# Kernel tuning notes

Hardware: AMD Instinct MI355X
Metric: run time of the kernel (lower is better)

Reference implementation:

```python
import jax, jax.numpy as jnp
import numpy as np

B, N, C = 16, 4096, 64
M, K, R = 1024, 32, 0.2
EPS = 1e-5  # BatchNorm eps (eval mode: running_mean=0, running_var=1)


def setup_inputs() -> dict:
    key = jax.random.key(0)
    ks = jax.random.split(key, 8)
    s = 0.05
    return {
        "points": jax.random.normal(ks[0], (B, 3, N), dtype=jnp.float32),
        "features": jax.random.normal(ks[1], (B, C, N), dtype=jnp.float32),
        "w1": jax.random.normal(ks[2], (64, 3 + C), dtype=jnp.float32) * s,
        "b1": jnp.zeros((64,), jnp.float32),
        "g1": jnp.ones((64,), jnp.float32),
        "be1": jnp.zeros((64,), jnp.float32),
        "w2": jax.random.normal(ks[3], (64, 64), dtype=jnp.float32) * s,
        "b2": jnp.zeros((64,), jnp.float32),
        "g2": jnp.ones((64,), jnp.float32),
        "be2": jnp.zeros((64,), jnp.float32),
        "w3": jax.random.normal(ks[4], (128, 64), dtype=jnp.float32) * s,
        "b3": jnp.zeros((128,), jnp.float32),
        "g3": jnp.ones((128,), jnp.float32),
        "be3": jnp.zeros((128,), jnp.float32),
    }


def farthest_point_sampling(pts, m):
    """pts: [B,N,3] -> indices [B,m] (iterative FPS, first point = index 0)."""
    b, n, _ = pts.shape

    def step(carry, _):
        dist, last = carry  # dist [b,n], last [b]
        lastp = jnp.take_along_axis(pts, last[:, None, None], axis=1)  # [b,1,3]
        d = jnp.sum((pts - lastp) ** 2, axis=-1)  # [b,n]
        dist = jnp.minimum(dist, d)
        nxt = jnp.argmax(dist, axis=1).astype(jnp.int32)
        return (dist, nxt), last

    init = (jnp.full((b, n), 1e10, pts.dtype), jnp.zeros((b,), jnp.int32))
    _, idx = jax.lax.scan(step, init, None, length=m)
    return idx.T  # [b,m]


def ball_query(pts, centroids, k, radius):
    """pts [B,N,3], centroids [B,M,3] -> neighbor indices [B,M,K].
    Takes the first k points (by index) within radius; pads with the first hit,
    matching the PointNet++ CUDA ball_query semantics."""
    n = pts.shape[1]
    p2 = jnp.sum(pts ** 2, -1)  # [B,N]
    c2 = jnp.sum(centroids ** 2, -1)  # [B,M]
    d2 = c2[:, :, None] + p2[:, None, :] - 2.0 * jnp.einsum("bmd,bnd->bmn", centroids, pts)
    ar = jnp.arange(n, dtype=jnp.int32)
    key = jnp.where(d2 <= radius * radius, ar[None, None, :], n)  # [B,M,N]
    idx = jnp.sort(key, axis=-1)[..., :k]  # first k in-radius indices (or n)
    first = idx[..., :1]  # centroid itself is always a hit (d2=0)
    idx = jnp.where(idx < n, idx, first)
    return jnp.clip(idx, 0, n - 1)


def _mlp_block(x, w, bias, g, be):
    # 1x1 Conv2d + BatchNorm (eval: mean=0, var=1) + ReLU, x: [B,M,K,Cin]
    y = jnp.einsum("oc,bmkc->bmko", w, x) + bias
    y = y * (g / jnp.sqrt(1.0 + EPS)) + be
    return jax.nn.relu(y)


def reference(points, features, w1, b1, g1, be1, w2, b2, g2, be2, w3, b3, g3, be3):
    pts = jnp.transpose(points, (0, 2, 1))  # [B,N,3]
    feats = jnp.transpose(features, (0, 2, 1))  # [B,N,C]
    b = pts.shape[0]

    cidx = farthest_point_sampling(pts, M)  # [B,M]
    bidx = jnp.arange(b)[:, None]
    cent = pts[bidx, cidx]  # [B,M,3]

    nidx = ball_query(pts, cent, K, R)  # [B,M,K]
    bidx2 = jnp.arange(b)[:, None, None]
    gpts = pts[bidx2, nidx]  # [B,M,K,3]
    gfeat = feats[bidx2, nidx]  # [B,M,K,C]
    local = gpts - cent[:, :, None, :]  # local coords
    x = jnp.concatenate([local, gfeat], axis=-1)  # [B,M,K,3+C]

    x = _mlp_block(x, w1, b1, g1, be1)
    x = _mlp_block(x, w2, b2, g2, be2)
    x = _mlp_block(x, w3, b3, g3, be3)

    out = jnp.max(x, axis=2)  # max over K samples -> [B,M,Cout]
    centroids = jnp.transpose(cent, (0, 2, 1))  # [B,3,M]
    out = jnp.transpose(out, (0, 2, 1))  # [B,Cout,M]
    return centroids, out
```

## Files before the change

kernel.cpp:

```cpp
#include <hip/hip_runtime.h>
#include <math.h>

#define NPTS 4096
#define MC   1024
#define KNB  32

typedef __attribute__((ext_vector_type(8))) short bf16x8;
typedef __attribute__((ext_vector_type(4))) float f32x4;

__device__ __forceinline__ unsigned short f2bf(float f) {
  unsigned int u = __float_as_uint(f);
  u = u + 0x7fffu + ((u >> 16) & 1u);
  return (unsigned short)(u >> 16);
}

template <int CTRL>
__device__ __forceinline__ unsigned long long dpp_kmax(unsigned long long k) {
  int lo = (int)(unsigned int)k;
  int hi = (int)(unsigned int)(k >> 32);
  int lo2 = __builtin_amdgcn_update_dpp(lo, lo, CTRL, 0xF, 0xF, false);
  int hi2 = __builtin_amdgcn_update_dpp(hi, hi, CTRL, 0xF, 0xF, false);
  unsigned long long k2 =
      ((unsigned long long)(unsigned int)hi2 << 32) | (unsigned int)lo2;
  return (k2 > k) ? k2 : k;
}

struct FpsShared {
  float sx[NPTS], sy[NPTS], sz[NPTS];
  unsigned long long skey[2][8];
  float slog[3][MC];
};
struct TransShared {
  float tile[64][129];
};

__global__ __launch_bounds__(512, 1) void fused_pre(
    const float* __restrict__ points, const float* __restrict__ feats,
    const float* __restrict__ w1, const float* __restrict__ w2,
    const float* __restrict__ w3,
    unsigned short* __restrict__ featsT, unsigned short* __restrict__ wpack,
    float* __restrict__ out_cent) {
  __shared__ union { FpsShared f; TransShared tr; } S;
  const int blk = blockIdx.x;
  const int t = threadIdx.x;

  if (blk < 16) {
    const int b = blk;
    const int w = t >> 6;
    const float* pb = points + (size_t)b * 3 * NPTS;

    float fx[8], fy[8], fz[8], dist[8];
#pragma unroll
    for (int k = 0; k < 2; ++k) {
      float4 X = ((const float4*)pb)[k * 512 + t];
      float4 Y = ((const float4*)(pb + NPTS))[k * 512 + t];
      float4 Z = ((const float4*)(pb + 2 * NPTS))[k * 512 + t];
      ((float4*)S.f.sx)[k * 512 + t] = X;
      ((float4*)S.f.sy)[k * 512 + t] = Y;
      ((float4*)S.f.sz)[k * 512 + t] = Z;
      fx[k * 4 + 0] = X.x; fx[k * 4 + 1] = X.y; fx[k * 4 + 2] = X.z; fx[k * 4 + 3] = X.w;
      fy[k * 4 + 0] = Y.x; fy[k * 4 + 1] = Y.y; fy[k * 4 + 2] = Y.z; fy[k * 4 + 3] = Y.w;
      fz[k * 4 + 0] = Z.x; fz[k * 4 + 1] = Z.y; fz[k * 4 + 2] = Z.z; fz[k * 4 + 3] = Z.w;
    }
#pragma unroll
    for (int j = 0; j < 8; ++j) dist[j] = 1e10f;
    __syncthreads();

    float lx = S.f.sx[0], ly = S.f.sy[0], lz = S.f.sz[0];

    for (int i = 0; i < MC; ++i) {
      if (t == 0) { S.f.slog[0][i] = lx; S.f.slog[1][i] = ly; S.f.slog[2][i] = lz; }
      if (i == MC - 1) break;

      float m = -1.0f;
      int mj = 0;
#pragma unroll
      for (int j = 0; j < 8; ++j) {
        float dx = __fsub_rn(fx[j], lx);
        float dy = __fsub_rn(fy[j], ly);
        float dz = __fsub_rn(fz[j], lz);
        float d  = __fadd_rn(__fadd_rn(__fmul_rn(dx, dx), __fmul_rn(dy, dy)), __fmul_rn(dz, dz));
        float dm = fminf(dist[j], d);
        dist[j] = dm;
        bool gt = dm > m;
        m  = gt ? dm : m;
        mj = gt ? j : mj;
      }

      const int gidx = ((mj >> 2) << 11) | (t << 2) | (mj & 3);
      unsigned long long key =
          ((unsigned long long)__float_as_uint(m) << 32) | (unsigned int)~gidx;
      key = dpp_kmax<0x111>(key);
      key = dpp_kmax<0x112>(key);
      key = dpp_kmax<0x114>(key);
      key = dpp_kmax<0x118>(key);
      key = dpp_kmax<0x142>(key);
      key = dpp_kmax<0x143>(key);

      const int nb = i & 1;
      if ((t & 63) == 63) S.f.skey[nb][w] = key;
      __syncthreads();

      unsigned long long km = S.f.skey[nb][0];
#pragma unroll
      for (int r = 1; r < 8; ++r) {
        unsigned long long kr = S.f.skey[nb][r];
        km = (kr > km) ? kr : km;
      }
      const int sel = (int)(~(unsigned int)km);
      lx = S.f.sx[sel]; ly = S.f.sy[sel]; lz = S.f.sz[sel];
    }
    __syncthreads();
    float* oc = out_cent + (size_t)b * 3 * MC;
#pragma unroll
    for (int k = 0; k < 6; ++k) {
      int idx = t + k * 512;
      oc[idx] = ((const float*)S.f.slog)[idx];
    }
  } else if (blk < 16 + 512) {
    const int rel = blk - 16;
    const int b = rel >> 5;
    const int n0 = (rel & 31) * 128;
    const float* src = feats + (size_t)b * 64 * NPTS;
    {
      const int n = t & 127, cbase = t >> 7;
#pragma unroll
      for (int j = 0; j < 16; ++j) {
        int cc = cbase + j * 4;
        S.tr.tile[cc][n] = src[(size_t)cc * NPTS + n0 + n];
      }
    }
    __syncthreads();
    {
      const int cc = t & 63, nbase = t >> 6;
      unsigned short* dst = featsT + ((size_t)b * NPTS + n0) * 64;
#pragma unroll
      for (int j = 0; j < 16; ++j) {
        int n = nbase + j * 8;
        dst[(size_t)n * 64 + cc] = f2bf(S.tr.tile[cc][n]);
      }
    }
  } else {
    const int f = (blk - (16 + 512)) * 8 + (t >> 6);
    const int lane = t & 63;
    if (f < 36) {
      int layer, kt, nt;
      if (f < 12)      { layer = 0; kt = f >> 2;        nt = f & 3; }
      else if (f < 20) { layer = 1; kt = (f - 12) >> 2; nt = (f - 12) & 3; }
      else             { layer = 2; kt = (f - 20) >> 3; nt = (f - 20) & 7; }
      const int o = nt * 16 + (lane & 15);
      unsigned short* dst = wpack + ((size_t)f * 64 + lane) * 8;
#pragma unroll
      for (int j = 0; j < 8; ++j) {
        int k = kt * 32 + (lane >> 4) * 8 + j;
        float x = 0.0f;
        if (layer == 0)      { if (k < 67) { int cin = (k < 64) ? (k + 3) : (k - 64); x = w1[o * 67 + cin]; } }
        else if (layer == 1) { x = w2[o * 64 + k]; }
        else                 { x = w3[o * 64 + k]; }
        dst[j] = f2bf(x);
      }
    }
  }
}

__global__ __launch_bounds__(256) void ball_query_kernel(const float* __restrict__ points,
                                                         const float* __restrict__ cent,
                                                         int* __restrict__ nidx) {
  __shared__ float sx[NPTS], sy[NPTS], sz[NPTS];
  __shared__ int lists[4][KNB];
  const int b  = blockIdx.x >> 4;
  const int cb = blockIdx.x & 15;
  const int t = threadIdx.x;
  const float* pb = points + (size_t)b * 3 * NPTS;
#pragma unroll
  for (int j = 0; j < 4; ++j) {
    int i4 = t + j * 256;
    ((float4*)sx)[i4] = ((const float4*)pb)[i4];
    ((float4*)sy)[i4] = ((const float4*)(pb + NPTS))[i4];
    ((float4*)sz)[i4] = ((const float4*)(pb + 2 * NPTS))[i4];
  }
  __syncthreads();
  const int w = t >> 6, lane = t & 63;
  const float R2 = (float)(0.2 * 0.2);
  const float* cbp = cent + (size_t)b * 3 * MC;
  for (int cm = 0; cm < 16; ++cm) {
    const int m  = cb * 64 + w * 16 + cm;
    const int bm = b * MC + m;
    const float cx = cbp[m], cy = cbp[MC + m], cz = cbp[2 * MC + m];
    const float c2 = __fadd_rn(__fadd_rn(__fmul_rn(cx, cx), __fmul_rn(cy, cy)), __fmul_rn(cz, cz));
    int cnt = 0;
    for (int ch = 0; ch < 64; ++ch) {
      const int n = ch * 64 + lane;
      float x = sx[n], y = sy[n], z = sz[n];
      float p2  = __fadd_rn(__fadd_rn(__fmul_rn(x, x),  __fmul_rn(y, y)),  __fmul_rn(z, z));
      float dot = __fadd_rn(__fadd_rn(__fmul_rn(cx, x), __fmul_rn(cy, y)), __fmul_rn(cz, z));
      float d2  = __fsub_rn(__fadd_rn(c2, p2), __fmul_rn(2.0f, dot));
      bool hit = (d2 <= R2);
      unsigned long long msk = __ballot(hit);
      if (hit) {
        int pos = cnt + __popcll(msk & ((1ull << lane) - 1ull));
        if (pos < KNB) lists[w][pos] = n;
      }
      cnt += __popcll(msk);
      if (cnt >= KNB) break;
    }
    if (lane < KNB) {
      int first = lists[w][0];
      int v = (lane < cnt) ? lists[w][lane] : first;
      nidx[(size_t)bm * KNB + lane] = v;
    }
  }
}

__global__ __launch_bounds__(256) void mlp_kernel(
    const float* __restrict__ points,
    const float* __restrict__ cent,
    const int* __restrict__ nidx,
    const unsigned short* __restrict__ featsT,
    const unsigned short* __restrict__ wpack,
    const float* __restrict__ b1, const float* __restrict__ g1, const float* __restrict__ be1,
    const float* __restrict__ b2, const float* __restrict__ g2, const float* __restrict__ be2,
    const float* __restrict__ b3, const float* __restrict__ g3, const float* __restrict__ be3,
    float* __restrict__ out) {
  __shared__ __align__(16) unsigned short Hs[4][2][32 * 72];
  __shared__ __align__(16) float obuf[128 * 20];
  const int t = threadIdx.x;
  const int w = t >> 6, lane = t & 63;
  const int r = lane & 15, q = lane >> 4;
  const float inv_s = 1.0f / sqrtf(1.0f + 1e-5f);

  float pb1[4], ps1[4], pe1[4], pb2[4], ps2[4], pe2[4], pb3[8], ps3[8], pe3[8];
#pragma unroll
  for (int nt = 0; nt < 4; ++nt) {
    int o = nt * 16 + r;
    pb1[nt] = b1[o]; ps1[nt] = g1[o] * inv_s; pe1[nt] = be1[o];
    pb2[nt] = b2[o]; ps2[nt] = g2[o] * inv_s; pe2[nt] = be2[o];
  }
#pragma unroll
  for (int nt = 0; nt < 8; ++nt) {
    int o = nt * 16 + r;
    pb3[nt] = b3[o]; ps3[nt] = g3[o] * inv_s; pe3[nt] = be3[o];
  }
  const int bm0 = blockIdx.x * 16;
  const int b   = bm0 >> 10;
  const int m0  = bm0 & 1023;
  const float* ptsb = points + (size_t)b * 3 * NPTS;
  const float* cbp  = cent + (size_t)b * 3 * MC;

  for (int it = 0; it < 4; ++it) {
    const int ml = it * 4 + w;
    const int bm = bm0 + ml;
    const int m  = bm & 1023;
    const int n0 = nidx[(size_t)bm * KNB + r];
    const int n1 = nidx[(size_t)bm * KNB + 16 + r];
    const float cx = cbp[m], cy = cbp[MC + m], cz = cbp[2 * MC + m];

    bf16x8 aF[2][2];
#pragma unroll
    for (int mt = 0; mt < 2; ++mt) {
      int n = mt ? n1 : n0;
      const unsigned short* rowp = featsT + ((size_t)b * NPTS + n) * 64 + q * 8;
      aF[mt][0] = *(const bf16x8*)(rowp);
      aF[mt][1] = *(const bf16x8*)(rowp + 32);
    }
    bf16x8 aL[2];
#pragma unroll
    for (int mt = 0; mt < 2; ++mt) {
      bf16x8 a = {0, 0, 0, 0, 0, 0, 0, 0};
      if (q == 0) {
        int n = mt ? n1 : n0;
        a[0] = (short)f2bf(ptsb[n] - cx);
        a[1] = (short)f2bf(ptsb[NPTS + n] - cy);
        a[2] = (short)f2bf(ptsb[2 * NPTS + n] - cz);
      }
      aL[mt] = a;
    }
    f32x4 acc1[2][4];
#pragma unroll
    for (int mt = 0; mt < 2; ++mt)
#pragma unroll
      for (int nt = 0; nt < 4; ++nt) acc1[mt][nt] = (f32x4){0.f, 0.f, 0.f, 0.f};
#pragma unroll
    for (int kt = 0; kt < 3; ++kt) {
#pragma unroll
      for (int nt = 0; nt < 4; ++nt) {
        bf16x8 wf = *(const bf16x8*)(wpack + ((size_t)(kt * 4 + nt) * 64 + lane) * 8);
#pragma unroll
        for (int mt = 0; mt < 2; ++mt) {
          bf16x8 a = (kt < 2) ? aF[mt][kt] : aL[mt];
          acc1[mt][nt] = __builtin_amdgcn_mfma_f32_16x16x32_bf16(a, wf, acc1[mt][nt], 0, 0, 0);
        }
      }
    }
#pragma unroll
    for (int mt = 0; mt < 2; ++mt)
#pragma unroll
      for (int nt = 0; nt < 4; ++nt)
#pragma unroll
        for (int rr = 0; rr < 4; ++rr) {
          float y = (acc1[mt][nt][rr] + pb1[nt]) * ps1[nt] + pe1[nt];
          y = fmaxf(y, 0.0f);
          Hs[w][0][(mt * 16 + q * 4 + rr) * 72 + nt * 16 + r] = f2bf(y);
        }
    __threadfence_block();

    f32x4 acc2[2][4];
#pragma unroll
    for (int mt = 0; mt < 2; ++mt)
#pragma unroll
      for (int nt = 0; nt < 4; ++nt) acc2[mt][nt] = (f32x4){0.f, 0.f, 0.f, 0.f};
#pragma unroll
    for (int kt = 0; kt < 2; ++kt) {
      bf16x8 a0 = *(const bf16x8*)&Hs[w][0][(0 * 16 + r) * 72 + kt * 32 + q * 8];
      bf16x8 a1 = *(const bf16x8*)&Hs[w][0][(1 * 16 + r) * 72 + kt * 32 + q * 8];
#pragma unroll
      for (int nt = 0; nt < 4; ++nt) {
        bf16x8 wf = *(const bf16x8*)(wpack + ((size_t)(12 + kt * 4 + nt) * 64 + lane) * 8);
        acc2[0][nt] = __builtin_amdgcn_mfma_f32_16x16x32_bf16(a0, wf, acc2[0][nt], 0, 0, 0);
        acc2[1][nt] = __builtin_amdgcn_mfma_f32_16x16x32_bf16(a1, wf, acc2[1][nt], 0, 0, 0);
      }
    }
#pragma unroll
    for (int mt = 0; mt < 2; ++mt)
#pragma unroll
      for (int nt = 0; nt < 4; ++nt)
#pragma unroll
        for (int rr = 0; rr < 4; ++rr) {
          float y = (acc2[mt][nt][rr] + pb2[nt]) * ps2[nt] + pe2[nt];
          y = fmaxf(y, 0.0f);
          Hs[w][1][(mt * 16 + q * 4 + rr) * 72 + nt * 16 + r] = f2bf(y);
        }
    __threadfence_block();

    f32x4 acc3[2][8];
#pragma unroll
    for (int mt = 0; mt < 2; ++mt)
#pragma unroll
      for (int nt = 0; nt < 8; ++nt) acc3[mt][nt] = (f32x4){0.f, 0.f, 0.f, 0.f};
#pragma unroll
    for (int kt = 0; kt < 2; ++kt) {
      bf16x8 a0 = *(const bf16x8*)&Hs[w][1][(0 * 16 + r) * 72 + kt * 32 + q * 8];
      bf16x8 a1 = *(const bf16x8*)&Hs[w][1][(1 * 16 + r) * 72 + kt * 32 + q * 8];
#pragma unroll
      for (int nt = 0; nt < 8; ++nt) {
        bf16x8 wf = *(const bf16x8*)(wpack + ((size_t)(20 + kt * 8 + nt) * 64 + lane) * 8);
        acc3[0][nt] = __builtin_amdgcn_mfma_f32_16x16x32_bf16(a0, wf, acc3[0][nt], 0, 0, 0);
        acc3[1][nt] = __builtin_amdgcn_mfma_f32_16x16x32_bf16(a1, wf, acc3[1][nt], 0, 0, 0);
      }
    }
#pragma unroll
    for (int nt = 0; nt < 8; ++nt) {
      float pm = 0.0f;
#pragma unroll
      for (int mt = 0; mt < 2; ++mt)
#pragma unroll
        for (int rr = 0; rr < 4; ++rr) {
          float y = (acc3[mt][nt][rr] + pb3[nt]) * ps3[nt] + pe3[nt];
          y = fmaxf(y, 0.0f);
          pm = fmaxf(pm, y);
        }
      pm = fmaxf(pm, __shfl_xor(pm, 16));
      pm = fmaxf(pm, __shfl_xor(pm, 32));
      if (q == 0) obuf[(nt * 16 + r) * 20 + ml] = pm;
    }
    __threadfence_block();
  }
  __syncthreads();
  {
    const int ch = t >> 1, mh = (t & 1) * 8;
    float4 u0 = *(const float4*)&obuf[ch * 20 + mh];
    float4 u1 = *(const float4*)&obuf[ch * 20 + mh + 4];
    float* outp = out + ((size_t)b * 128 + ch) * 1024 + m0 + mh;
    *(float4*)(outp)     = u0;
    *(float4*)(outp + 4) = u1;
  }
}

extern "C" void kernel_launch(void* const* d_in, const int* in_sizes, int n_in,
                              void* d_out, int out_size, void* d_ws, size_t ws_size,
                              hipStream_t stream) {
  (void)in_sizes; (void)n_in; (void)out_size; (void)ws_size;
  const float* points   = (const float*)d_in[0];
  const float* features = (const float*)d_in[1];
  const float* w1  = (const float*)d_in[2];
  const float* b1  = (const float*)d_in[3];
  const float* g1  = (const float*)d_in[4];
  const float* be1 = (const float*)d_in[5];
  const float* w2  = (const float*)d_in[6];
  const float* b2  = (const float*)d_in[7];
  const float* g2  = (const float*)d_in[8];
  const float* be2 = (const float*)d_in[9];
  const float* w3  = (const float*)d_in[10];
  const float* b3  = (const float*)d_in[11];
  const float* g3  = (const float*)d_in[12];
  const float* be3 = (const float*)d_in[13];

  float* outc = (float*)d_out;
  float* outf = outc + 16 * 3 * 1024;

  char* ws = (char*)d_ws;
  int*            nidx    = (int*)(ws);
  unsigned short* featsT  = (unsigned short*)(ws + 0x200000);
  unsigned short* wpack   = (unsigned short*)(ws + 0xA00000);

  fused_pre<<<16 + 512 + 5, 512, 0, stream>>>(points, features, w1, w2, w3,
                                              featsT, wpack, outc);
  ball_query_kernel<<<256, 256, 0, stream>>>(points, outc, nidx);
  mlp_kernel<<<1024, 256, 0, stream>>>(points, outc, nidx, featsT, wpack,
                                       b1, g1, be1, b2, g2, be2, b3, g3, be3, outf);
}
```

Measured before the change: 1.120 ms.

## Interleave two FPS batches per block with float DPP max and ballot argmax

Each FPS block now processes two batch elements at once, interleaving their independent distance updates and reductions so the latency-bound serial loop has more instruction-level parallelism and one barrier serves both. The 64-bit key DPP reduction becomes a 32-bit float max followed by ballots to recover the lowest matching index. Shared-memory point copies are dropped and the next centroid is fetched from global memory with uniform scalar indices. In exchange, each thread holds twice the registers and each iteration issues a global load whose latency may land on the critical path.

```diff
diff --git a/kernel.cpp b/kernel.cpp
--- a/kernel.cpp
+++ b/kernel.cpp
@@ -15,20 +15,14 @@
 }
 
 template <int CTRL>
-__device__ __forceinline__ unsigned long long dpp_kmax(unsigned long long k) {
-  int lo = (int)(unsigned int)k;
-  int hi = (int)(unsigned int)(k >> 32);
-  int lo2 = __builtin_amdgcn_update_dpp(lo, lo, CTRL, 0xF, 0xF, false);
-  int hi2 = __builtin_amdgcn_update_dpp(hi, hi, CTRL, 0xF, 0xF, false);
-  unsigned long long k2 =
-      ((unsigned long long)(unsigned int)hi2 << 32) | (unsigned int)lo2;
-  return (k2 > k) ? k2 : k;
+__device__ __forceinline__ float dpp_max(float v) {
+  int o = __builtin_amdgcn_update_dpp(__float_as_int(v), __float_as_int(v), CTRL, 0xF, 0xF, false);
+  return fmaxf(v, __int_as_float(o));
 }
 
 struct FpsShared {
-  float sx[NPTS], sy[NPTS], sz[NPTS];
-  unsigned long long skey[2][8];
-  float slog[3][MC];
+  unsigned long long skey[2][2][8];
+  float slog[2][3][MC];
 };
 struct TransShared {
   float tile[64][129];
@@ -44,81 +38,160 @@
   const int blk = blockIdx.x;
   const int t = threadIdx.x;
 
-  if (blk < 16) {
-    const int b = blk;
-    const int w = t >> 6;
-    const float* pb = points + (size_t)b * 3 * NPTS;
-
-    float fx[8], fy[8], fz[8], dist[8];
+  if (blk < 8) {
+    const int w = t >> 6, lane = t & 63;
+    const float* pA = points + (size_t)(2 * blk) * 3 * NPTS;
+    const float* pB = pA + 3 * NPTS;
+
+    float Ax[8], Ay[8], Az[8], Ad[8];
+    float Bx[8], By[8], Bz[8], Bd[8];
 #pragma unroll
     for (int k = 0; k < 2; ++k) {
-      float4 X = ((const float4*)pb)[k * 512 + t];
-      float4 Y = ((const float4*)(pb + NPTS))[k * 512 + t];
-      float4 Z = ((const float4*)(pb + 2 * NPTS))[k * 512 + t];
-      ((float4*)S.f.sx)[k * 512 + t] = X;
-      ((float4*)S.f.sy)[k * 512 + t] = Y;
-      ((float4*)S.f.sz)[k * 512 + t] = Z;
-      fx[k * 4 + 0] = X.x; fx[k * 4 + 1] = X.y; fx[k * 4 + 2] = X.z; fx[k * 4 + 3] = X.w;
-      fy[k * 4 + 0] = Y.x; fy[k * 4 + 1] = Y.y; fy[k * 4 + 2] = Y.z; fy[k * 4 + 3] = Y.w;
-      fz[k * 4 + 0] = Z.x; fz[k * 4 + 1] = Z.y; fz[k * 4 + 2] = Z.z; fz[k * 4 + 3] = Z.w;
-    }
-#pragma unroll
-    for (int j = 0; j < 8; ++j) dist[j] = 1e10f;
+      float4 X = ((const float4*)pA)[k * 512 + t];
+      float4 Y = ((const float4*)(pA + NPTS))[k * 512 + t];
+      float4 Z = ((const float4*)(pA + 2 * NPTS))[k * 512 + t];
+      Ax[k * 4 + 0] = X.x; Ax[k * 4 + 1] = X.y; Ax[k * 4 + 2] = X.z; Ax[k * 4 + 3] = X.w;
+      Ay[k * 4 + 0] = Y.x; Ay[k * 4 + 1] = Y.y; Ay[k * 4 + 2] = Y.z; Ay[k * 4 + 3] = Y.w;
+      Az[k * 4 + 0] = Z.x; Az[k * 4 + 1] = Z.y; Az[k * 4 + 2] = Z.z; Az[k * 4 + 3] = Z.w;
+      float4 X2 = ((const float4*)pB)[k * 512 + t];
+      float4 Y2 = ((const float4*)(pB + NPTS))[k * 512 + t];
+      float4 Z2 = ((const float4*)(pB + 2 * NPTS))[k * 512 + t];
+      Bx[k * 4 + 0] = X2.x; Bx[k * 4 + 1] = X2.y; Bx[k * 4 + 2] = X2.z; Bx[k * 4 + 3] = X2.w;
+      By[k * 4 + 0] = Y2.x; By[k * 4 + 1] = Y2.y; By[k * 4 + 2] = Y2.z; By[k * 4 + 3] = Y2.w;
+      Bz[k * 4 + 0] = Z2.x; Bz[k * 4 + 1] = Z2.y; Bz[k * 4 + 2] = Z2.z; Bz[k * 4 + 3] = Z2.w;
+    }
+#pragma unroll
+    for (int j = 0; j < 8; ++j) { Ad[j] = 1e10f; Bd[j] = 1e10f; }
+
+    float lxA = pA[0], lyA = pA[NPTS], lzA = pA[2 * NPTS];
+    float lxB = pB[0], lyB = pB[NPTS], lzB = pB[2 * NPTS];
+
+    for (int i = 0; i < MC; ++i) {
+      if (t == 0)        { S.f.slog[0][0][i] = lxA; S.f.slog[0][1][i] = lyA; S.f.slog[0][2][i] = lzA; }
+      else if (t == 256) { S.f.slog[1][0][i] = lxB; S.f.slog[1][1][i] = lyB; S.f.slog[1][2][i] = lzB; }
+      if (i == MC - 1) break;
+
+      float mA = -1.0f, mB = -1.0f;
+#pragma unroll
+      for (int j = 0; j < 8; ++j) {
+        float dxA = __fsub_rn(Ax[j], lxA);
+        float dyA = __fsub_rn(Ay[j], lyA);
+        float dzA = __fsub_rn(Az[j], lzA);
+        float dA  = __fadd_rn(__fadd_rn(__fmul_rn(dxA, dxA), __fmul_rn(dyA, dyA)), __fmul_rn(dzA, dzA));
+        float dmA = fminf(Ad[j], dA);
+        Ad[j] = dmA;
+        mA = fmaxf(mA, dmA);
+        float dxB = __fsub_rn(Bx[j], lxB);
+        float dyB = __fsub_rn(By[j], lyB);
+        float dzB = __fsub_rn(Bz[j], lzB);
+        float dB  = __fadd_rn(__fadd_rn(__fmul_rn(dxB, dxB), __fmul_rn(dyB, dyB)), __fmul_rn(dzB, dzB));
+        float dmB = fminf(Bd[j], dB);
+        Bd[j] = dmB;
+        mB = fmaxf(mB, dmB);
+      }
+
+      float ra = mA, rb = mB;
+      ra = dpp_max<0x111>(ra); rb = dpp_max<0x111>(rb);
+      ra = dpp_max<0x112>(ra); rb = dpp_max<0x112>(rb);
+      ra = dpp_max<0x114>(ra); rb = dpp_max<0x114>(rb);
+      ra = dpp_max<0x118>(ra); rb = dpp_max<0x118>(rb);
+      ra = dpp_max<0x142>(ra); rb = dpp_max<0x142>(rb);
+      ra = dpp_max<0x143>(ra); rb = dpp_max<0x143>(rb);
+      const float wvA = __int_as_float(__builtin_amdgcn_readlane(__float_as_int(ra), 63));
+      const float wvB = __int_as_float(__builtin_amdgcn_readlane(__float_as_int(rb), 63));
+
+      unsigned long long mkA[2][4], mkB[2][4];
+#pragma unroll
+      for (int k = 0; k < 2; ++k) {
+        mkA[k][0] = __ballot(Ad[k * 4 + 0] == wvA);
+        mkA[k][1] = __ballot(Ad[k * 4 + 1] == wvA);
+        mkA[k][2] = __ballot(Ad[k * 4 + 2] == wvA);
+        mkA[k][3] = __ballot(Ad[k * 4 + 3] == wvA);
+        mkB[k][0] = __ballot(Bd[k * 4 + 0] == wvB);
+        mkB[k][1] = __ballot(Bd[k * 4 + 1] == wvB);
+        mkB[k][2] = __ballot(Bd[k * 4 + 2] == wvB);
+        mkB[k][3] = __ballot(Bd[k * 4 + 3] == wvB);
+      }
+      const int par = i & 1;
+      {
+        unsigned long long s0 = 0, s1 = 0, s2 = 0, s3 = 0, anyk = 0;
+        int sk = -1;
+#pragma unroll
+        for (int k = 0; k < 2; ++k) {
+          unsigned long long a = mkA[k][0] | mkA[k][1] | mkA[k][2] | mkA[k][3];
+          if (sk < 0 && a != 0ull) {
+            sk = k; anyk = a;
+            s0 = mkA[k][0]; s1 = mkA[k][1]; s2 = mkA[k][2]; s3 = mkA[k][3];
+          }
+        }
+        const int l = __builtin_ctzll(anyk);
+        const unsigned long long bit = 1ull << l;
+        const int c = (s0 & bit) ? 0 : (s1 & bit) ? 1 : (s2 & bit) ? 2 : 3;
+        const int selIdx = sk * 2048 + 256 * w + 4 * l + c;
+        if (lane == 0)
+          S.f.skey[0][par][w] =
+              ((unsigned long long)__float_as_uint(wvA) << 32) | (unsigned int)~selIdx;
+      }
+      {
+        unsigned long long s0 = 0, s1 = 0, s2 = 0, s3 = 0, anyk = 0;
+        int sk = -1;
+#pragma unroll
+        for (int k = 0; k < 2; ++k) {
+          unsigned long long a = mkB[k][0] | mkB[k][1] | mkB[k][2] | mkB[k][3];
+          if (sk < 0 && a != 0ull) {
+            sk = k; anyk = a;
+            s0 = mkB[k][0]; s1 = mkB[k][1]; s2 = mkB[k][2]; s3 = mkB[k][3];
+          }
+        }
+        const int l = __builtin_ctzll(anyk);
+        const unsigned long long bit = 1ull << l;
+        const int c = (s0 & bit) ? 0 : (s1 & bit) ? 1 : (s2 & bit) ? 2 : 3;
+        const int selIdx = sk * 2048 + 256 * w + 4 * l + c;
+        if (lane == 0)
+          S.f.skey[1][par][w] =
+              ((unsigned long long)__float_as_uint(wvB) << 32) | (unsigned int)~selIdx;
+      }
+      __syncthreads();
+
+      int selA, selB;
+      {
+        unsigned long long k0 = S.f.skey[0][par][0], k1 = S.f.skey[0][par][1];
+        unsigned long long k2 = S.f.skey[0][par][2], k3 = S.f.skey[0][par][3];
+        unsigned long long k4 = S.f.skey[0][par][4], k5 = S.f.skey[0][par][5];
+        unsigned long long k6 = S.f.skey[0][par][6], k7 = S.f.skey[0][par][7];
+        unsigned long long ka = (k0 > k1) ? k0 : k1, kb = (k2 > k3) ? k2 : k3;
+        unsigned long long kc = (k4 > k5) ? k4 : k5, kd = (k6 > k7) ? k6 : k7;
+        unsigned long long ke = (ka > kb) ? ka : kb, kf = (kc > kd) ? kc : kd;
+        unsigned long long km = (ke > kf) ? ke : kf;
+        selA = (int)(~(unsigned int)km);
+      }
+      {
+        unsigned long long k0 = S.f.skey[1][par][0], k1 = S.f.skey[1][par][1];
+        unsigned long long k2 = S.f.skey[1][par][2], k3 = S.f.skey[1][par][3];
+        unsigned long long k4 = S.f.skey[1][par][4], k5 = S.f.skey[1][par][5];
+        unsigned long long k6 = S.f.skey[1][par][6], k7 = S.f.skey[1][par][7];
+        unsigned long long ka = (k0 > k1) ? k0 : k1, kb = (k2 > k3) ? k2 : k3;
+        unsigned long long kc = (k4 > k5) ? k4 : k5, kd = (k6 > k7) ? k6 : k7;
+        unsigned long long ke = (ka > kb) ? ka : kb, kf = (kc > kd) ? kc : kd;
+        unsigned long long km = (ke > kf) ? ke : kf;
+        selB = (int)(~(unsigned int)km);
+      }
+      const int sA = __builtin_amdgcn_readfirstlane(selA);
+      const int sB = __builtin_amdgcn_readfirstlane(selB);
+      lxA = pA[sA]; lyA = pA[NPTS + sA]; lzA = pA[2 * NPTS + sA];
+      lxB = pB[sB]; lyB = pB[NPTS + sB]; lzB = pB[2 * NPTS + sB];
+    }
     __syncthreads();
-
-    float lx = S.f.sx[0], ly = S.f.sy[0], lz = S.f.sz[0];
-
-    for (int i = 0; i < MC; ++i) {
-      if (t == 0) { S.f.slog[0][i] = lx; S.f.slog[1][i] = ly; S.f.slog[2][i] = lz; }
-      if (i == MC - 1) break;
-
-      float m = -1.0f;
-      int mj = 0;
-#pragma unroll
-      for (int j = 0; j < 8; ++j) {
-        float dx = __fsub_rn(fx[j], lx);
-        float dy = __fsub_rn(fy[j], ly);
-        float dz = __fsub_rn(fz[j], lz);
-        float d  = __fadd_rn(__fadd_rn(__fmul_rn(dx, dx), __fmul_rn(dy, dy)), __fmul_rn(dz, dz));
-        float dm = fminf(dist[j], d);
-        dist[j] = dm;
-        bool gt = dm > m;
-        m  = gt ? dm : m;
-        mj = gt ? j : mj;
-      }
-
-      const int gidx = ((mj >> 2) << 11) | (t << 2) | (mj & 3);
-      unsigned long long key =
-          ((unsigned long long)__float_as_uint(m) << 32) | (unsigned int)~gidx;
-      key = dpp_kmax<0x111>(key);
-      key = dpp_kmax<0x112>(key);
-      key = dpp_kmax<0x114>(key);
-      key = dpp_kmax<0x118>(key);
-      key = dpp_kmax<0x142>(key);
-      key = dpp_kmax<0x143>(key);
-
-      const int nb = i & 1;
-      if ((t & 63) == 63) S.f.skey[nb][w] = key;
-      __syncthreads();
-
-      unsigned long long km = S.f.skey[nb][0];
-#pragma unroll
-      for (int r = 1; r < 8; ++r) {
-        unsigned long long kr = S.f.skey[nb][r];
-        km = (kr > km) ? kr : km;
-      }
-      const int sel = (int)(~(unsigned int)km);
-      lx = S.f.sx[sel]; ly = S.f.sy[sel]; lz = S.f.sz[sel];
-    }
-    __syncthreads();
-    float* oc = out_cent + (size_t)b * 3 * MC;
+    float* ocA = out_cent + (size_t)(2 * blk) * 3 * MC;
+    float* ocB = ocA + 3 * MC;
 #pragma unroll
     for (int k = 0; k < 6; ++k) {
       int idx = t + k * 512;
-      oc[idx] = ((const float*)S.f.slog)[idx];
-    }
-  } else if (blk < 16 + 512) {
-    const int rel = blk - 16;
+      ocA[idx] = ((const float*)S.f.slog[0])[idx];
+      ocB[idx] = ((const float*)S.f.slog[1])[idx];
+    }
+  } else if (blk < 8 + 512) {
+    const int rel = blk - 8;
     const int b = rel >> 5;
     const int n0 = (rel & 31) * 128;
     const float* src = feats + (size_t)b * 64 * NPTS;
@@ -141,7 +214,7 @@
       }
     }
   } else {
-    const int f = (blk - (16 + 512)) * 8 + (t >> 6);
+    const int f = (blk - (8 + 512)) * 8 + (t >> 6);
     const int lane = t & 63;
     if (f < 36) {
       int layer, kt, nt;
@@ -403,8 +476,8 @@
   unsigned short* featsT  = (unsigned short*)(ws + 0x200000);
   unsigned short* wpack   = (unsigned short*)(ws + 0xA00000);
 
-  fused_pre<<<16 + 512 + 5, 512, 0, stream>>>(points, features, w1, w2, w3,
-                                              featsT, wpack, outc);
+  fused_pre<<<8 + 512 + 5, 512, 0, stream>>>(points, features, w1, w2, w3,
+                                             featsT, wpack, outc);
   ball_query_kernel<<<256, 256, 0, stream>>>(points, outc, nidx);
   mlp_kernel<<<1024, 256, 0, stream>>>(points, outc, nidx, featsT, wpack,
                                        b1, g1, be1, b2, g2, be2, b3, g3, be3, outf);
```

New measurement: 1.941 ms. +73.3%, slower.
